# Performance work log

Measured on AMD Instinct MI355X. Metric: run time of the kernel, lower is better.

Reference implementation:

```python
import jax, jax.numpy as jnp
import numpy as np
from jax import lax

DIM = 1024
DIM_INNER = 2048  # int(dim * expansion_factor)


def log_g(x):
    # log-space g(x): where(x>=0, log(relu(x)+0.5), -softplus(-x))
    return jnp.where(x >= 0, jnp.log(jax.nn.relu(x) + 0.5), -jax.nn.softplus(-x))


def heinsen_associative_scan_log(log_coeffs, log_values):
    # parallel log-space linear recurrence over the sequence axis (axis=1)
    a_star = jnp.cumsum(log_coeffs, axis=1)
    log_h0_plus_b_star = lax.cumlogsumexp(log_values - a_star, axis=1)
    return a_star + log_h0_plus_b_star


def setup_inputs() -> dict:
    key = jax.random.key(0)
    k_x, k_w1, k_w2 = jax.random.split(key, 3)
    x = jax.random.normal(k_x, (4, 4096, DIM), dtype=jnp.float32)
    # Linear(dim, 2*dim_inner, bias=False): store as [in, out] for x @ W
    W_hg = jax.random.normal(k_w1, (DIM, 2 * DIM_INNER), dtype=jnp.float32) * (1.0 / np.sqrt(DIM))
    W_out = jax.random.normal(k_w2, (DIM_INNER, DIM), dtype=jnp.float32) * (1.0 / np.sqrt(DIM_INNER))
    return {"x": x, "W_hg": W_hg, "W_out": W_out}


def reference(x, W_hg, W_out):
    # x: [b, s, dim]
    hg = jnp.einsum('bsd,de->bse', x, W_hg)  # [b, s, 2*dim_inner]
    hidden, gate = jnp.split(hg, 2, axis=-1)
    log_coeffs = -jax.nn.softplus(gate)        # log(1 - z)
    log_z = -jax.nn.softplus(-gate)            # log z
    log_values = log_z + log_g(hidden)
    log_h = heinsen_associative_scan_log(log_coeffs, log_values)  # [b, s, dim_inner]
    out = jnp.exp(log_h)
    return jnp.einsum('bse,ed->bsd', out, W_out)
```

## Files before the change

kernel.cpp:

```cpp
#include <hip/hip_runtime.h>
#include <cmath>

#define DIM 1024
#define DIM_INNER 2048
#define BATCH 4
#define SEQ 4096
#define MTOT (BATCH * SEQ)
#define CHUNK 32
#define NCHUNK (SEQ / CHUNK)

typedef __bf16 bf16x8 __attribute__((ext_vector_type(8)));
typedef short short8_t __attribute__((ext_vector_type(8)));
typedef float floatx4 __attribute__((ext_vector_type(4)));
typedef unsigned short u16x4 __attribute__((ext_vector_type(4)));
typedef unsigned int uint4_t __attribute__((ext_vector_type(4)));
typedef float float4_t __attribute__((ext_vector_type(4)));
typedef unsigned short ushort_t;

__device__ __forceinline__ unsigned short f2bf(float f) {
  unsigned int u = __builtin_bit_cast(unsigned int, f);
  u += 0x7fffu + ((u >> 16) & 1u);
  return (unsigned short)(u >> 16);
}
__device__ __forceinline__ float bflo2f(unsigned int u) {
  return __builtin_bit_cast(float, u << 16);
}
__device__ __forceinline__ float bfhi2f(unsigned int u) {
  return __builtin_bit_cast(float, u & 0xffff0000u);
}

__device__ __forceinline__ void lclv_fast(float h, float g, float& lc, float& lv) {
  float eg = __expf(-fabsf(g));
  float sp = fmaxf(g, 0.f) + __logf(1.f + eg);
  lc = -sp;
  float eh = __expf(h);
  float t  = (h >= 0.f) ? (h + 0.5f) : (1.f + eh);
  float lt = __logf(t);
  float lg = (h >= 0.f) ? lt : (h - lt);
  lv = g + lc + lg;
}
__device__ __forceinline__ float logaddexp_f(float a, float b) {
  float m = fmaxf(a, b);
  return m + __logf(1.f + __expf(-fabsf(a - b)));
}

__device__ __forceinline__ void async_copy16(const ushort_t* g, ushort_t* l) {
  __builtin_amdgcn_global_load_lds(
      (const __attribute__((address_space(1))) void*)g,
      (__attribute__((address_space(3))) void*)l, 16, 0, 0);
}

__global__ __launch_bounds__(256) void convert_f32_bf16(
    const float* __restrict__ src, ushort_t* __restrict__ dst) {
  int i = blockIdx.x * 256 + threadIdx.x;
  float4 v = ((const float4*)src)[i];
  u16x4 o = {f2bf(v.x), f2bf(v.y), f2bf(v.z), f2bf(v.w)};
  ((u16x4*)dst)[i] = o;
}

__global__ __launch_bounds__(256) void transpose_f32_bf16(
    const float* __restrict__ src, ushort_t* __restrict__ dst, int K, int N) {
  __shared__ float tile[32][33];
  int tx = threadIdx.x & 31, ty = threadIdx.x >> 5;
  int n0 = blockIdx.x * 32, k0 = blockIdx.y * 32;
#pragma unroll
  for (int i = 0; i < 4; i++) {
    int k = ty + i * 8;
    tile[k][tx] = src[(size_t)(k0 + k) * N + n0 + tx];
  }
  __syncthreads();
#pragma unroll
  for (int i = 0; i < 4; i++) {
    int r = ty + i * 8;
    dst[(size_t)(n0 + r) * K + k0 + tx] = f2bf(tile[tx][r]);
  }
}

#define G1_BK 64
#define G1_NT (DIM / G1_BK)

__global__ __launch_bounds__(512, 2) void gemm1_fused(
    const ushort_t* __restrict__ Xbf, const ushort_t* __restrict__ Wt,
    unsigned int* __restrict__ LCLV) {
  __shared__ __align__(16) ushort_t lds[81920];

  const int tid = threadIdx.x;
  const int wv = tid >> 6;
  const int lane = tid & 63;
  const int wr = wv >> 2;
  const int wc = wv & 3;
  const int l15 = lane & 15;
  const int quad = lane >> 4;
  const int n0 = blockIdx.x * 128;
  const int m0 = blockIdx.y * 256;

  floatx4 acc[8][4];
#pragma unroll
  for (int i = 0; i < 8; i++)
#pragma unroll
    for (int j = 0; j < 4; j++) acc[i][j] = (floatx4){0.f, 0.f, 0.f, 0.f};

  bf16x8 aF[4][2], bF[2][2];

  auto stageA = [&](int kt, int half, int buf) {
#pragma unroll
    for (int L = 0; L < 2; L++) {
      int e = L * 512 + tid;
      int row = e >> 3, slot = e & 7;
      const ushort_t* src = Xbf + (size_t)(m0 + half * 128 + row) * DIM +
                            kt * 64 + ((slot ^ (row & 7)) << 3);
      async_copy16(src, lds + (buf * 2 + half) * 8192 + e * 8);
    }
  };
  auto stageB = [&](int kt, int half, int buf) {
#pragma unroll
    for (int L = 0; L < 2; L++) {
      int e = L * 512 + tid;
      int row = e >> 3, slot = e & 7;
      int br = half * 128 + row;
      int grow = n0 + ((br >> 6) << 5) + (br & 31) + ((br & 32) ? DIM_INNER : 0);
      const ushort_t* src = Wt + (size_t)grow * DIM +
                            kt * 64 + ((slot ^ (row & 7)) << 3);
      async_copy16(src, lds + 49152 + (buf * 2 + half) * 8192 + e * 8);
    }
  };
  auto readA = [&](int buf, int mf, int ks) -> bf16x8 {
    int r = mf * 16 + l15;
    const ushort_t* p = lds + (buf * 2 + wr) * 8192 + r * 64 +
                        ((((ks << 2) | quad) ^ (r & 7)) << 3);
    return __builtin_bit_cast(bf16x8, *(const short8_t*)p);
  };
  auto readB = [&](int buf, int nf, int ks) -> bf16x8 {
    int br = wc * 64 + nf * 16 + l15;
    int half = br >> 7, r = br & 127;
    const ushort_t* p = lds + 49152 + (buf * 2 + half) * 8192 + r * 64 +
                        ((((ks << 2) | quad) ^ (r & 7)) << 3);
    return __builtin_bit_cast(bf16x8, *(const short8_t*)p);
  };
  auto mmaQ = [&](int mb, int nb) {
#pragma unroll
    for (int mf = 0; mf < 4; mf++)
#pragma unroll
      for (int nf = 0; nf < 2; nf++)
#pragma unroll
        for (int ks = 0; ks < 2; ks++)
          acc[mb + mf][nb + nf] = __builtin_amdgcn_mfma_f32_16x16x32_bf16(
              aF[mf][ks], bF[nf][ks], acc[mb + mf][nb + nf], 0, 0, 0);
  };

  stageA(0, 0, 0); stageA(0, 1, 0);
  stageB(0, 0, 0); stageB(0, 1, 0);
  stageA(1, 0, 1); stageA(1, 1, 1);
  asm volatile("s_waitcnt vmcnt(4)" ::: "memory");
  __builtin_amdgcn_s_barrier();

  int bufA = 0, bufB = 0, bufAn = 2, bufBn = 1;
  for (int u = 0; u < G1_NT; u++) {
    const int kb = (u + 1 < G1_NT) ? u + 1 : G1_NT - 1;
    const int ka = (u + 2 < G1_NT) ? u + 2 : G1_NT - 1;

#pragma unroll
    for (int mf = 0; mf < 4; mf++)
#pragma unroll
      for (int ks = 0; ks < 2; ks++) aF[mf][ks] = readA(bufA, mf, ks);
#pragma unroll
    for (int nf = 0; nf < 2; nf++)
#pragma unroll
      for (int ks = 0; ks < 2; ks++) bF[nf][ks] = readB(bufB, nf, ks);
    stageB(kb, 0, bufBn);
    __builtin_amdgcn_s_barrier();
    asm volatile("s_waitcnt lgkmcnt(0)" ::: "memory");
    __builtin_amdgcn_sched_barrier(0);
    __builtin_amdgcn_s_setprio(1);
    mmaQ(0, 0);
    __builtin_amdgcn_s_setprio(0);
    __builtin_amdgcn_s_barrier();

#pragma unroll
    for (int nf = 0; nf < 2; nf++)
#pragma unroll
      for (int ks = 0; ks < 2; ks++) bF[nf][ks] = readB(bufB, nf + 2, ks);
    stageB(kb, 1, bufBn);
    __builtin_amdgcn_s_barrier();
    asm volatile("s_waitcnt lgkmcnt(0)" ::: "memory");
    __builtin_amdgcn_sched_barrier(0);
    __builtin_amdgcn_s_setprio(1);
    mmaQ(0, 2);
    __builtin_amdgcn_s_setprio(0);
    __builtin_amdgcn_s_barrier();

#pragma unroll
    for (int mf = 0; mf < 4; mf++)
#pragma unroll
      for (int ks = 0; ks < 2; ks++) aF[mf][ks] = readA(bufA, mf + 4, ks);
    stageA(ka, 0, bufAn);
    __builtin_amdgcn_s_barrier();
    asm volatile("s_waitcnt lgkmcnt(0)" ::: "memory");
    __builtin_amdgcn_sched_barrier(0);
    __builtin_amdgcn_s_setprio(1);
    mmaQ(4, 2);
    __builtin_amdgcn_s_setprio(0);
    __builtin_amdgcn_s_barrier();

#pragma unroll
    for (int nf = 0; nf < 2; nf++)
#pragma unroll
      for (int ks = 0; ks < 2; ks++) bF[nf][ks] = readB(bufB, nf, ks);
    stageA(ka, 1, bufAn);
    asm volatile("s_waitcnt vmcnt(4)" ::: "memory");
    __builtin_amdgcn_s_barrier();
    asm volatile("s_waitcnt lgkmcnt(0)" ::: "memory");
    __builtin_amdgcn_sched_barrier(0);
    __builtin_amdgcn_s_setprio(1);
    mmaQ(4, 0);
    __builtin_amdgcn_s_setprio(0);
    __builtin_amdgcn_s_barrier();

    bufA = (bufA == 2) ? 0 : bufA + 1;
    bufAn = (bufAn == 2) ? 0 : bufAn + 1;
    bufB ^= 1; bufBn ^= 1;
  }

#pragma unroll
  for (int mf = 0; mf < 8; mf++)
#pragma unroll
    for (int j = 0; j < 2; j++) {
      int col = n0 + wc * 32 + j * 16 + l15;
#pragma unroll
      for (int r = 0; r < 4; r++) {
        int row = m0 + wr * 128 + mf * 16 + quad * 4 + r;
        float lc, lv;
        lclv_fast(acc[mf][j][r], acc[mf][j + 2][r], lc, lv);
        unsigned int pk = ((unsigned int)f2bf(lv) << 16) | (unsigned int)f2bf(lc);
        LCLV[(size_t)row * DIM_INNER + col] = pk;
      }
    }
}

__global__ __launch_bounds__(256) void scan_phase1(
    const unsigned int* __restrict__ LCLV,
    float* __restrict__ Asum, float* __restrict__ Lend, int nbch) {
  const int EQ = DIM_INNER / 4;
  int tid = blockIdx.x * 256 + threadIdx.x;
  int ep = tid % EQ;
  int tmp = tid / EQ;
  int c = tmp % NCHUNK;
  int bz = tmp / NCHUNK;
  size_t base4 = ((size_t)bz * SEQ + (size_t)c * CHUNK) * EQ + ep;
  const uint4_t* L4 = (const uint4_t*)LCLV;

  float4_t asum = {0.f, 0.f, 0.f, 0.f};
  float4_t logh = {-INFINITY, -INFINITY, -INFINITY, -INFINITY};
#pragma unroll 4
  for (int t = 0; t < CHUNK; t++) {
    uint4_t u = L4[base4 + (size_t)t * EQ];
#pragma unroll
    for (int k = 0; k < 4; k++) {
      float lc = bflo2f(u[k]), lv = bfhi2f(u[k]);
      asum[k] += lc;
      logh[k] = logaddexp_f(lc + logh[k], lv);
    }
  }
  size_t sidx = ((size_t)c * nbch + (size_t)bz * DIM_INNER) / 4 + ep;
  ((float4_t*)Asum)[sidx] = asum;
  ((float4_t*)Lend)[sidx] = logh;
}

__global__ __launch_bounds__(256) void scan_phase2(
    float* Asum, const float* __restrict__ Lend, int nbch) {
  int ch = blockIdx.x * 256 + threadIdx.x;
  float p = -INFINITY;
  for (int c = 0; c < NCHUNK; c++) {
    float a = Asum[(size_t)c * nbch + ch];
    float le = Lend[(size_t)c * nbch + ch];
    Asum[(size_t)c * nbch + ch] = p;
    p = logaddexp_f(a + p, le);
  }
}

__global__ __launch_bounds__(256) void scan_phase3(
    const unsigned int* __restrict__ LCLV, const float* __restrict__ P,
    ushort_t* __restrict__ H, int nbch) {
  const int EQ = DIM_INNER / 4;
  int tid = blockIdx.x * 256 + threadIdx.x;
  int ep = tid % EQ;
  int tmp = tid / EQ;
  int c = tmp % NCHUNK;
  int bz = tmp / NCHUNK;
  size_t base4 = ((size_t)bz * SEQ + (size_t)c * CHUNK) * EQ + ep;
  const uint4_t* L4 = (const uint4_t*)LCLV;
  u16x4* H4 = (u16x4*)H;

  size_t pidx = ((size_t)c * nbch + (size_t)bz * DIM_INNER) / 4 + ep;
  float4_t logh = ((const float4_t*)P)[pidx];
#pragma unroll 4
  for (int t = 0; t < CHUNK; t++) {
    uint4_t u = L4[base4 + (size_t)t * EQ];
    u16x4 hv;
#pragma unroll
    for (int k = 0; k < 4; k++) {
      float lc = bflo2f(u[k]), lv = bfhi2f(u[k]);
      logh[k] = logaddexp_f(lc + logh[k], lv);
      hv[k] = f2bf(__expf(logh[k]));
    }
    H4[base4 + (size_t)t * EQ] = hv;
  }
}

__global__ __launch_bounds__(256) void gemm2(
    const ushort_t* __restrict__ Hbf, const ushort_t* __restrict__ Wot,
    float* __restrict__ OUT) {
  __shared__ __align__(16) ushort_t As[128 * 32];
  __shared__ __align__(16) ushort_t Bs[128 * 32];

  const int tid = threadIdx.x;
  const int wave = tid >> 6;
  const int lane = tid & 63;
  const int n0 = blockIdx.x * 128;
  const int m0 = blockIdx.y * 128;
  const int l15 = lane & 15;
  const int quad = lane >> 4;
  const int wr = wave >> 1, wc = wave & 1;
  const int lrow = lane >> 2;
  const int lkof = (lane & 3) * 8;

  floatx4 acc[4][4];
#pragma unroll
  for (int i = 0; i < 4; i++)
#pragma unroll
    for (int j = 0; j < 4; j++) acc[i][j] = (floatx4){0.f, 0.f, 0.f, 0.f};

  for (int k0 = 0; k0 < DIM_INNER; k0 += 32) {
    __syncthreads();
#pragma unroll
    for (int p = 0; p < 2; p++) {
      int u = wave + p * 4;
      async_copy16(Hbf + (size_t)(m0 + u * 16 + lrow) * DIM_INNER + k0 + lkof,
                   As + u * 512);
      async_copy16(Wot + (size_t)(n0 + u * 16 + lrow) * DIM_INNER + k0 + lkof,
                   Bs + u * 512);
    }
    __syncthreads();

    bf16x8 af[4], bf[4];
#pragma unroll
    for (int i = 0; i < 4; i++) {
      short8_t sa = *(const short8_t*)(As + (size_t)(wr * 64 + i * 16 + l15) * 32 + quad * 8);
      af[i] = __builtin_bit_cast(bf16x8, sa);
      short8_t sb = *(const short8_t*)(Bs + (size_t)(wc * 64 + i * 16 + l15) * 32 + quad * 8);
      bf[i] = __builtin_bit_cast(bf16x8, sb);
    }
#pragma unroll
    for (int i = 0; i < 4; i++)
#pragma unroll
      for (int j = 0; j < 4; j++)
        acc[i][j] = __builtin_amdgcn_mfma_f32_16x16x32_bf16(af[i], bf[j], acc[i][j], 0, 0, 0);
  }

#pragma unroll
  for (int i = 0; i < 4; i++)
#pragma unroll
    for (int j = 0; j < 4; j++) {
      int col = n0 + wc * 64 + j * 16 + l15;
#pragma unroll
      for (int r = 0; r < 4; r++) {
        int row = m0 + wr * 64 + i * 16 + quad * 4 + r;
        OUT[(size_t)row * DIM + col] = acc[i][j][r];
      }
    }
}

extern "C" void kernel_launch(void* const* d_in, const int* in_sizes, int n_in,
                              void* d_out, int out_size, void* d_ws, size_t ws_size,
                              hipStream_t stream) {
  const float* X = (const float*)d_in[0];
  const float* Whg = (const float*)d_in[1];
  const float* Wout = (const float*)d_in[2];
  float* out = (float*)d_out;

  ushort_t* Xbf = (ushort_t*)d_ws;
  ushort_t* Whg_t = Xbf + (size_t)MTOT * DIM;
  ushort_t* Wout_t = Whg_t + (size_t)(2 * DIM_INNER) * DIM;
  char* pp = (char*)(Wout_t + (size_t)DIM * DIM_INNER);

  const size_t fixed_bytes = (size_t)MTOT * DIM * 2 +
                             (size_t)2 * DIM_INNER * DIM * 2 +
                             (size_t)DIM * DIM_INNER * 2;
  const size_t per_batch = (size_t)SEQ * DIM_INNER * 4 +
                           (size_t)SEQ * DIM_INNER * 2 +
                           2 * (size_t)DIM_INNER * NCHUNK * 4;
  int nb = 4;
  while (nb > 1 && fixed_bytes + (size_t)nb * per_batch > ws_size) nb >>= 1;
  const int npass = BATCH / nb;

  convert_f32_bf16<<<(MTOT * DIM / 4) / 256, 256, 0, stream>>>(X, Xbf);
  transpose_f32_bf16<<<dim3(2 * DIM_INNER / 32, DIM / 32), 256, 0, stream>>>(
      Whg, Whg_t, DIM, 2 * DIM_INNER);
  transpose_f32_bf16<<<dim3(DIM / 32, DIM_INNER / 32), 256, 0, stream>>>(
      Wout, Wout_t, DIM_INNER, DIM);

  for (int pass = 0; pass < npass; pass++) {
    const int b0 = pass * nb;
    const int nrows = nb * SEQ;
    const int nbch = nb * DIM_INNER;

    unsigned int* LCLV = (unsigned int*)pp;
    ushort_t* Hbf = (ushort_t*)(LCLV + (size_t)nb * SEQ * DIM_INNER);
    float* Asum = (float*)(Hbf + (size_t)nb * SEQ * DIM_INNER);
    float* Lend = Asum + (size_t)nb * DIM_INNER * NCHUNK;

    gemm1_fused<<<dim3(DIM_INNER / 128, nrows / 256), 512, 0, stream>>>(
        Xbf + (size_t)b0 * SEQ * DIM, Whg_t, LCLV);
    scan_phase1<<<(nbch / 4 * NCHUNK) / 256, 256, 0, stream>>>(LCLV, Asum, Lend, nbch);
    scan_phase2<<<nbch / 256, 256, 0, stream>>>(Asum, Lend, nbch);
    scan_phase3<<<(nbch / 4 * NCHUNK) / 256, 256, 0, stream>>>(LCLV, Asum, Hbf, nbch);
    gemm2<<<dim3(DIM / 128, nrows / 128), 256, 0, stream>>>(
        Hbf, Wout_t, out + (size_t)b0 * SEQ * DIM);
  }
}
```

Before: 493.0 us.

## Pipeline GEMM1 LDS reads with incremental waits and rebuild GEMM2 on same schedule

GEMM1's main loop now precomputes global and LDS addresses. It splits fragment loads so MFMAs start after partial lgkmcnt waits instead of draining all LDS reads, and peels the last two iterations to drop redundant prefetches. GEMM2 is rewritten from a simple single-buffered 128x128 kernel into a 256x256, 512-thread, multi-buffered swizzled kernel that reuses the same schedule. This raises data reuse and overlaps memory with compute. The cost is higher register and LDS pressure and fewer blocks for GEMM2.

```diff
diff --git a/kernel.cpp b/kernel.cpp
--- a/kernel.cpp
+++ b/kernel.cpp
@@ -16,6 +16,14 @@
 typedef unsigned int uint4_t __attribute__((ext_vector_type(4)));
 typedef float float4_t __attribute__((ext_vector_type(4)));
 typedef unsigned short ushort_t;
+
+template <int N> struct IC { static constexpr int v = N; };
+template <bool B> struct BC { static constexpr bool v = B; };
+
+#define LGKM_SB(n) do { asm volatile("s_waitcnt lgkmcnt(" #n ")" ::: "memory"); \
+                        __builtin_amdgcn_sched_barrier(0); } while (0)
+#define SCHED0() __builtin_amdgcn_sched_barrier(0)
+#define SBAR() __builtin_amdgcn_s_barrier()
 
 __device__ __forceinline__ unsigned short f2bf(float f) {
   unsigned int u = __builtin_bit_cast(unsigned int, f);
@@ -76,8 +84,8 @@
   }
 }
 
-#define G1_BK 64
-#define G1_NT (DIM / G1_BK)
+#define G1_NT (DIM / 64)
+#define G2_NT (DIM_INNER / 64)
 
 __global__ __launch_bounds__(512, 2) void gemm1_fused(
     const ushort_t* __restrict__ Xbf, const ushort_t* __restrict__ Wt,
@@ -94,132 +102,163 @@
   const int n0 = blockIdx.x * 128;
   const int m0 = blockIdx.y * 256;
 
-  floatx4 acc[8][4];
-#pragma unroll
-  for (int i = 0; i < 8; i++)
-#pragma unroll
-    for (int j = 0; j < 4; j++) acc[i][j] = (floatx4){0.f, 0.f, 0.f, 0.f};
-
-  bf16x8 aF[4][2], bF[2][2];
-
-  auto stageA = [&](int kt, int half, int buf) {
-#pragma unroll
-    for (int L = 0; L < 2; L++) {
-      int e = L * 512 + tid;
-      int row = e >> 3, slot = e & 7;
-      const ushort_t* src = Xbf + (size_t)(m0 + half * 128 + row) * DIM +
-                            kt * 64 + ((slot ^ (row & 7)) << 3);
-      async_copy16(src, lds + (buf * 2 + half) * 8192 + e * 8);
-    }
-  };
-  auto stageB = [&](int kt, int half, int buf) {
-#pragma unroll
-    for (int L = 0; L < 2; L++) {
-      int e = L * 512 + tid;
-      int row = e >> 3, slot = e & 7;
+  int aSrc[2][2], bSrc[2][2];
+  int dstE[2];
+#pragma unroll
+  for (int L = 0; L < 2; L++) {
+    int e = L * 512 + tid;
+    int row = e >> 3, slot = e & 7;
+    int sw = (slot ^ (row & 7)) << 3;
+    dstE[L] = e * 8;
+#pragma unroll
+    for (int half = 0; half < 2; half++) {
+      aSrc[half][L] = (m0 + half * 128 + row) * DIM + sw;
       int br = half * 128 + row;
       int grow = n0 + ((br >> 6) << 5) + (br & 31) + ((br & 32) ? DIM_INNER : 0);
-      const ushort_t* src = Wt + (size_t)grow * DIM +
-                            kt * 64 + ((slot ^ (row & 7)) << 3);
-      async_copy16(src, lds + 49152 + (buf * 2 + half) * 8192 + e * 8);
-    }
-  };
+      bSrc[half][L] = grow * DIM + sw;
+    }
+  }
+
+  auto stageA = [&](int kt, int half, int buf) {
+#pragma unroll
+    for (int L = 0; L < 2; L++)
+      async_copy16(Xbf + aSrc[half][L] + kt * 64,
+                   lds + buf * 16384 + half * 8192 + dstE[L]);
+  };
+  auto stageB = [&](int kt, int half, int buf) {
+#pragma unroll
+    for (int L = 0; L < 2; L++)
+      async_copy16(Wt + bSrc[half][L] + kt * 64,
+                   lds + 49152 + buf * 16384 + half * 8192 + dstE[L]);
+  };
+
+  const int swz0 = ((quad ^ (l15 & 7)) << 3);
+  const int swz1 = (((4 | quad) ^ (l15 & 7)) << 3);
+  const int aB0 = wr * 8192 + l15 * 64 + swz0;
+  const int aB1 = wr * 8192 + l15 * 64 + swz1;
+  const int bB0 = wc * 4096 + l15 * 64 + swz0;
+  const int bB1 = wc * 4096 + l15 * 64 + swz1;
+
   auto readA = [&](int buf, int mf, int ks) -> bf16x8 {
-    int r = mf * 16 + l15;
-    const ushort_t* p = lds + (buf * 2 + wr) * 8192 + r * 64 +
-                        ((((ks << 2) | quad) ^ (r & 7)) << 3);
+    const ushort_t* p = lds + buf * 16384 + (ks ? aB1 : aB0) + mf * 1024;
     return __builtin_bit_cast(bf16x8, *(const short8_t*)p);
   };
   auto readB = [&](int buf, int nf, int ks) -> bf16x8 {
-    int br = wc * 64 + nf * 16 + l15;
-    int half = br >> 7, r = br & 127;
-    const ushort_t* p = lds + 49152 + (buf * 2 + half) * 8192 + r * 64 +
-                        ((((ks << 2) | quad) ^ (r & 7)) << 3);
+    const ushort_t* p = lds + 49152 + buf * 16384 + (ks ? bB1 : bB0) + nf * 1024;
     return __builtin_bit_cast(bf16x8, *(const short8_t*)p);
   };
-  auto mmaQ = [&](int mb, int nb) {
-#pragma unroll
-    for (int mf = 0; mf < 4; mf++)
-#pragma unroll
-      for (int nf = 0; nf < 2; nf++)
-#pragma unroll
-        for (int ks = 0; ks < 2; ks++)
-          acc[mb + mf][nb + nf] = __builtin_amdgcn_mfma_f32_16x16x32_bf16(
-              aF[mf][ks], bF[nf][ks], acc[mb + mf][nb + nf], 0, 0, 0);
-  };
-
+
+  floatx4 acc[8][4];
+#pragma unroll
+  for (int i = 0; i < 8; i++)
+#pragma unroll
+    for (int j = 0; j < 4; j++) acc[i][j] = (floatx4){0.f, 0.f, 0.f, 0.f};
+
+  bf16x8 aF[4][2], b0F[2][2], b1F[2][2];
+
+  auto mma4 = [&](auto MA, auto MC, auto J, bf16x8 (&bX)[2][2]) {
+#pragma unroll
+    for (int jj = 0; jj < 2; jj++)
+#pragma unroll
+      for (int ks = 0; ks < 2; ks++)
+        acc[MC.v][J.v + jj] = __builtin_amdgcn_mfma_f32_16x16x32_bf16(
+            aF[MA.v][ks], bX[jj][ks], acc[MC.v][J.v + jj], 0, 0, 0);
+  };
+  auto mmaRow = [&](auto J, bf16x8 (&bvec)[2]) {
+#pragma unroll
+    for (int m = 0; m < 4; m++)
+#pragma unroll
+      for (int ks = 0; ks < 2; ks++)
+        acc[m][J.v] = __builtin_amdgcn_mfma_f32_16x16x32_bf16(
+            aF[m][ks], bvec[ks], acc[m][J.v], 0, 0, 0);
+  };
+
+  int bufA = 0, bufB = 0, bufAn = 2, bufBn = 1;
+
+  auto tileBody = [&](int kb, int ka, auto STB, auto STA, auto VMALL) {
+    aF[0][0] = readA(bufA, 0, 0); aF[0][1] = readA(bufA, 0, 1);
+    b0F[0][0] = readB(bufB, 0, 0); b0F[0][1] = readB(bufB, 0, 1);
+    b0F[1][0] = readB(bufB, 1, 0); b0F[1][1] = readB(bufB, 1, 1);
+    SCHED0();
+    aF[1][0] = readA(bufA, 1, 0); aF[1][1] = readA(bufA, 1, 1);
+    SCHED0();
+    aF[2][0] = readA(bufA, 2, 0); aF[2][1] = readA(bufA, 2, 1);
+    SCHED0();
+    aF[3][0] = readA(bufA, 3, 0); aF[3][1] = readA(bufA, 3, 1);
+    SCHED0();
+    if constexpr (STB.v) stageB(kb, 0, bufBn);
+    SBAR();
+    __builtin_amdgcn_s_setprio(1);
+    LGKM_SB(6); mma4(IC<0>{}, IC<0>{}, IC<0>{}, b0F);
+    LGKM_SB(4); mma4(IC<1>{}, IC<1>{}, IC<0>{}, b0F);
+    LGKM_SB(2); mma4(IC<2>{}, IC<2>{}, IC<0>{}, b0F);
+    LGKM_SB(0); mma4(IC<3>{}, IC<3>{}, IC<0>{}, b0F);
+    __builtin_amdgcn_s_setprio(0);
+    SBAR();
+
+    b1F[0][0] = readB(bufB, 2, 0); b1F[0][1] = readB(bufB, 2, 1);
+    SCHED0();
+    b1F[1][0] = readB(bufB, 3, 0); b1F[1][1] = readB(bufB, 3, 1);
+    SCHED0();
+    if constexpr (STB.v) stageB(kb, 1, bufBn);
+    SBAR();
+    __builtin_amdgcn_s_setprio(1);
+    LGKM_SB(2); mmaRow(IC<2>{}, b1F[0]);
+    LGKM_SB(0); mmaRow(IC<3>{}, b1F[1]);
+    __builtin_amdgcn_s_setprio(0);
+    SBAR();
+
+    aF[0][0] = readA(bufA, 4, 0); aF[0][1] = readA(bufA, 4, 1);
+    SCHED0();
+    aF[1][0] = readA(bufA, 5, 0); aF[1][1] = readA(bufA, 5, 1);
+    SCHED0();
+    aF[2][0] = readA(bufA, 6, 0); aF[2][1] = readA(bufA, 6, 1);
+    SCHED0();
+    aF[3][0] = readA(bufA, 7, 0); aF[3][1] = readA(bufA, 7, 1);
+    SCHED0();
+    if constexpr (STA.v) stageA(ka, 0, bufAn);
+    SBAR();
+    __builtin_amdgcn_s_setprio(1);
+    LGKM_SB(6); mma4(IC<0>{}, IC<4>{}, IC<2>{}, b1F);
+    LGKM_SB(4); mma4(IC<1>{}, IC<5>{}, IC<2>{}, b1F);
+    LGKM_SB(2); mma4(IC<2>{}, IC<6>{}, IC<2>{}, b1F);
+    LGKM_SB(0); mma4(IC<3>{}, IC<7>{}, IC<2>{}, b1F);
+    __builtin_amdgcn_s_setprio(0);
+    SBAR();
+
+    if constexpr (STA.v) stageA(ka, 1, bufAn);
+    SCHED0();
+    if constexpr (STA.v) {
+      asm volatile("s_waitcnt vmcnt(4)" ::: "memory");
+    } else if constexpr (VMALL.v) {
+      asm volatile("s_waitcnt vmcnt(0)" ::: "memory");
+    }
+    SBAR();
+    __builtin_amdgcn_s_setprio(1);
+    mma4(IC<0>{}, IC<4>{}, IC<0>{}, b0F);
+    mma4(IC<1>{}, IC<5>{}, IC<0>{}, b0F);
+    mma4(IC<2>{}, IC<6>{}, IC<0>{}, b0F);
+    mma4(IC<3>{}, IC<7>{}, IC<0>{}, b0F);
+    __builtin_amdgcn_s_setprio(0);
+    SBAR();
+  };
+
+  stageB(0, 0, 0); stageB(0, 1, 0);
   stageA(0, 0, 0); stageA(0, 1, 0);
-  stageB(0, 0, 0); stageB(0, 1, 0);
   stageA(1, 0, 1); stageA(1, 1, 1);
   asm volatile("s_waitcnt vmcnt(4)" ::: "memory");
-  __builtin_amdgcn_s_barrier();
-
-  int bufA = 0, bufB = 0, bufAn = 2, bufBn = 1;
-  for (int u = 0; u < G1_NT; u++) {
-    const int kb = (u + 1 < G1_NT) ? u + 1 : G1_NT - 1;
-    const int ka = (u + 2 < G1_NT) ? u + 2 : G1_NT - 1;
-
-#pragma unroll
-    for (int mf = 0; mf < 4; mf++)
-#pragma unroll
-      for (int ks = 0; ks < 2; ks++) aF[mf][ks] = readA(bufA, mf, ks);
-#pragma unroll
-    for (int nf = 0; nf < 2; nf++)
-#pragma unroll
-      for (int ks = 0; ks < 2; ks++) bF[nf][ks] = readB(bufB, nf, ks);
-    stageB(kb, 0, bufBn);
-    __builtin_amdgcn_s_barrier();
-    asm volatile("s_waitcnt lgkmcnt(0)" ::: "memory");
-    __builtin_amdgcn_sched_barrier(0);
-    __builtin_amdgcn_s_setprio(1);
-    mmaQ(0, 0);
-    __builtin_amdgcn_s_setprio(0);
-    __builtin_amdgcn_s_barrier();
-
-#pragma unroll
-    for (int nf = 0; nf < 2; nf++)
-#pragma unroll
-      for (int ks = 0; ks < 2; ks++) bF[nf][ks] = readB(bufB, nf + 2, ks);
-    stageB(kb, 1, bufBn);
-    __builtin_amdgcn_s_barrier();
-    asm volatile("s_waitcnt lgkmcnt(0)" ::: "memory");
-    __builtin_amdgcn_sched_barrier(0);
-    __builtin_amdgcn_s_setprio(1);
-    mmaQ(0, 2);
-    __builtin_amdgcn_s_setprio(0);
-    __builtin_amdgcn_s_barrier();
-
-#pragma unroll
-    for (int mf = 0; mf < 4; mf++)
-#pragma unroll
-      for (int ks = 0; ks < 2; ks++) aF[mf][ks] = readA(bufA, mf + 4, ks);
-    stageA(ka, 0, bufAn);
-    __builtin_amdgcn_s_barrier();
-    asm volatile("s_waitcnt lgkmcnt(0)" ::: "memory");
-    __builtin_amdgcn_sched_barrier(0);
-    __builtin_amdgcn_s_setprio(1);
-    mmaQ(4, 2);
-    __builtin_amdgcn_s_setprio(0);
-    __builtin_amdgcn_s_barrier();
-
-#pragma unroll
-    for (int nf = 0; nf < 2; nf++)
-#pragma unroll
-      for (int ks = 0; ks < 2; ks++) bF[nf][ks] = readB(bufB, nf, ks);
-    stageA(ka, 1, bufAn);
-    asm volatile("s_waitcnt vmcnt(4)" ::: "memory");
-    __builtin_amdgcn_s_barrier();
-    asm volatile("s_waitcnt lgkmcnt(0)" ::: "memory");
-    __builtin_amdgcn_sched_barrier(0);
-    __builtin_amdgcn_s_setprio(1);
-    mmaQ(4, 0);
-    __builtin_amdgcn_s_setprio(0);
-    __builtin_amdgcn_s_barrier();
-
+  SBAR();
+
+  for (int u = 0; u < G1_NT - 2; u++) {
+    tileBody(u + 1, u + 2, BC<true>{}, BC<true>{}, BC<false>{});
     bufA = (bufA == 2) ? 0 : bufA + 1;
     bufAn = (bufAn == 2) ? 0 : bufAn + 1;
     bufB ^= 1; bufBn ^= 1;
   }
+  tileBody(G1_NT - 1, 0, BC<true>{}, BC<false>{}, BC<true>{});
+  bufA = (bufA == 2) ? 0 : bufA + 1;
+  bufB ^= 1;
+  tileBody(0, 0, BC<false>{}, BC<false>{}, BC<false>{});
 
 #pragma unroll
   for (int mf = 0; mf < 8; mf++)
@@ -233,6 +272,190 @@
         lclv_fast(acc[mf][j][r], acc[mf][j + 2][r], lc, lv);
         unsigned int pk = ((unsigned int)f2bf(lv) << 16) | (unsigned int)f2bf(lc);
         LCLV[(size_t)row * DIM_INNER + col] = pk;
+      }
+    }
+}
+
+__global__ __launch_bounds__(512, 2) void gemm2(
+    const ushort_t* __restrict__ Hbf, const ushort_t* __restrict__ Wot,
+    float* __restrict__ OUT) {
+  __shared__ __align__(16) ushort_t lds[81920];
+
+  const int tid = threadIdx.x;
+  const int wv = tid >> 6;
+  const int lane = tid & 63;
+  const int wr = wv >> 2;
+  const int wc = wv & 3;
+  const int l15 = lane & 15;
+  const int quad = lane >> 4;
+  const int n0 = blockIdx.x * 256;
+  const int m0 = blockIdx.y * 256;
+
+  int aSrc[2][2], bSrc[2][2];
+  int dstE[2];
+#pragma unroll
+  for (int L = 0; L < 2; L++) {
+    int e = L * 512 + tid;
+    int row = e >> 3, slot = e & 7;
+    int sw = (slot ^ (row & 7)) << 3;
+    dstE[L] = e * 8;
+#pragma unroll
+    for (int half = 0; half < 2; half++) {
+      aSrc[half][L] = (m0 + half * 128 + row) * DIM_INNER + sw;
+      bSrc[half][L] = (n0 + half * 128 + row) * DIM_INNER + sw;
+    }
+  }
+
+  auto stageA = [&](int kt, int half, int buf) {
+#pragma unroll
+    for (int L = 0; L < 2; L++)
+      async_copy16(Hbf + aSrc[half][L] + kt * 64,
+                   lds + buf * 16384 + half * 8192 + dstE[L]);
+  };
+  auto stageB = [&](int kt, int half, int buf) {
+#pragma unroll
+    for (int L = 0; L < 2; L++)
+      async_copy16(Wot + bSrc[half][L] + kt * 64,
+                   lds + 49152 + buf * 16384 + half * 8192 + dstE[L]);
+  };
+
+  const int swz0 = ((quad ^ (l15 & 7)) << 3);
+  const int swz1 = (((4 | quad) ^ (l15 & 7)) << 3);
+  const int aB0 = wr * 8192 + l15 * 64 + swz0;
+  const int aB1 = wr * 8192 + l15 * 64 + swz1;
+  const int bB0 = wc * 4096 + l15 * 64 + swz0;
+  const int bB1 = wc * 4096 + l15 * 64 + swz1;
+
+  auto readA = [&](int buf, int mf, int ks) -> bf16x8 {
+    const ushort_t* p = lds + buf * 16384 + (ks ? aB1 : aB0) + mf * 1024;
+    return __builtin_bit_cast(bf16x8, *(const short8_t*)p);
+  };
+  auto readB = [&](int buf, int nf, int ks) -> bf16x8 {
+    const ushort_t* p = lds + 49152 + buf * 16384 + (ks ? bB1 : bB0) + nf * 1024;
+    return __builtin_bit_cast(bf16x8, *(const short8_t*)p);
+  };
+
+  floatx4 acc[8][4];
+#pragma unroll
+  for (int i = 0; i < 8; i++)
+#pragma unroll
+    for (int j = 0; j < 4; j++) acc[i][j] = (floatx4){0.f, 0.f, 0.f, 0.f};
+
+  bf16x8 aF[4][2], b0F[2][2], b1F[2][2];
+
+  auto mma4 = [&](auto MA, auto MC, auto J, bf16x8 (&bX)[2][2]) {
+#pragma unroll
+    for (int jj = 0; jj < 2; jj++)
+#pragma unroll
+      for (int ks = 0; ks < 2; ks++)
+        acc[MC.v][J.v + jj] = __builtin_amdgcn_mfma_f32_16x16x32_bf16(
+            aF[MA.v][ks], bX[jj][ks], acc[MC.v][J.v + jj], 0, 0, 0);
+  };
+  auto mmaRow = [&](auto J, bf16x8 (&bvec)[2]) {
+#pragma unroll
+    for (int m = 0; m < 4; m++)
+#pragma unroll
+      for (int ks = 0; ks < 2; ks++)
+        acc[m][J.v] = __builtin_amdgcn_mfma_f32_16x16x32_bf16(
+            aF[m][ks], bvec[ks], acc[m][J.v], 0, 0, 0);
+  };
+
+  int bufA = 0, bufB = 0, bufAn = 2, bufBn = 1;
+
+  auto tileBody = [&](int kb, int ka, auto STB, auto STA, auto VMALL) {
+    aF[0][0] = readA(bufA, 0, 0); aF[0][1] = readA(bufA, 0, 1);
+    b0F[0][0] = readB(bufB, 0, 0); b0F[0][1] = readB(bufB, 0, 1);
+    b0F[1][0] = readB(bufB, 1, 0); b0F[1][1] = readB(bufB, 1, 1);
+    SCHED0();
+    aF[1][0] = readA(bufA, 1, 0); aF[1][1] = readA(bufA, 1, 1);
+    SCHED0();
+    aF[2][0] = readA(bufA, 2, 0); aF[2][1] = readA(bufA, 2, 1);
+    SCHED0();
+    aF[3][0] = readA(bufA, 3, 0); aF[3][1] = readA(bufA, 3, 1);
+    SCHED0();
+    if constexpr (STB.v) stageB(kb, 0, bufBn);
+    SBAR();
+    __builtin_amdgcn_s_setprio(1);
+    LGKM_SB(6); mma4(IC<0>{}, IC<0>{}, IC<0>{}, b0F);
+    LGKM_SB(4); mma4(IC<1>{}, IC<1>{}, IC<0>{}, b0F);
+    LGKM_SB(2); mma4(IC<2>{}, IC<2>{}, IC<0>{}, b0F);
+    LGKM_SB(0); mma4(IC<3>{}, IC<3>{}, IC<0>{}, b0F);
+    __builtin_amdgcn_s_setprio(0);
+    SBAR();
+
+    b1F[0][0] = readB(bufB, 2, 0); b1F[0][1] = readB(bufB, 2, 1);
+    SCHED0();
+    b1F[1][0] = readB(bufB, 3, 0); b1F[1][1] = readB(bufB, 3, 1);
+    SCHED0();
+    if constexpr (STB.v) stageB(kb, 1, bufBn);
+    SBAR();
+    __builtin_amdgcn_s_setprio(1);
+    LGKM_SB(2); mmaRow(IC<2>{}, b1F[0]);
+    LGKM_SB(0); mmaRow(IC<3>{}, b1F[1]);
+    __builtin_amdgcn_s_setprio(0);
+    SBAR();
+
+    aF[0][0] = readA(bufA, 4, 0); aF[0][1] = readA(bufA, 4, 1);
+    SCHED0();
+    aF[1][0] = readA(bufA, 5, 0); aF[1][1] = readA(bufA, 5, 1);
+    SCHED0();
+    aF[2][0] = readA(bufA, 6, 0); aF[2][1] = readA(bufA, 6, 1);
+    SCHED0();
+    aF[3][0] = readA(bufA, 7, 0); aF[3][1] = readA(bufA, 7, 1);
+    SCHED0();
+    if constexpr (STA.v) stageA(ka, 0, bufAn);
+    SBAR();
+    __builtin_amdgcn_s_setprio(1);
+    LGKM_SB(6); mma4(IC<0>{}, IC<4>{}, IC<2>{}, b1F);
+    LGKM_SB(4); mma4(IC<1>{}, IC<5>{}, IC<2>{}, b1F);
+    LGKM_SB(2); mma4(IC<2>{}, IC<6>{}, IC<2>{}, b1F);
+    LGKM_SB(0); mma4(IC<3>{}, IC<7>{}, IC<2>{}, b1F);
+    __builtin_amdgcn_s_setprio(0);
+    SBAR();
+
+    if constexpr (STA.v) stageA(ka, 1, bufAn);
+    SCHED0();
+    if constexpr (STA.v) {
+      asm volatile("s_waitcnt vmcnt(4)" ::: "memory");
+    } else if constexpr (VMALL.v) {
+      asm volatile("s_waitcnt vmcnt(0)" ::: "memory");
+    }
+    SBAR();
+    __builtin_amdgcn_s_setprio(1);
+    mma4(IC<0>{}, IC<4>{}, IC<0>{}, b0F);
+    mma4(IC<1>{}, IC<5>{}, IC<0>{}, b0F);
+    mma4(IC<2>{}, IC<6>{}, IC<0>{}, b0F);
+    mma4(IC<3>{}, IC<7>{}, IC<0>{}, b0F);
+    __builtin_amdgcn_s_setprio(0);
+    SBAR();
+  };
+
+  stageB(0, 0, 0); stageB(0, 1, 0);
+  stageA(0, 0, 0); stageA(0, 1, 0);
+  stageA(1, 0, 1); stageA(1, 1, 1);
+  asm volatile("s_waitcnt vmcnt(4)" ::: "memory");
+  SBAR();
+
+  for (int u = 0; u < G2_NT - 2; u++) {
+    tileBody(u + 1, u + 2, BC<true>{}, BC<true>{}, BC<false>{});
+    bufA = (bufA == 2) ? 0 : bufA + 1;
+    bufAn = (bufAn == 2) ? 0 : bufAn + 1;
+    bufB ^= 1; bufBn ^= 1;
+  }
+  tileBody(G2_NT - 1, 0, BC<true>{}, BC<false>{}, BC<true>{});
+  bufA = (bufA == 2) ? 0 : bufA + 1;
+  bufB ^= 1;
+  tileBody(0, 0, BC<false>{}, BC<false>{}, BC<false>{});
+
+#pragma unroll
+  for (int mf = 0; mf < 8; mf++)
+#pragma unroll
+    for (int j = 0; j < 4; j++) {
+      int col = n0 + wc * 64 + (j >> 1) * 32 + (j & 1) * 16 + l15;
+#pragma unroll
+      for (int r = 0; r < 4; r++) {
+        int row = m0 + wr * 128 + mf * 16 + quad * 4 + r;
+        OUT[(size_t)row * DIM + col] = acc[mf][j][r];
       }
     }
 }
@@ -307,69 +530,6 @@
   }
 }
 
-__global__ __launch_bounds__(256) void gemm2(
-    const ushort_t* __restrict__ Hbf, const ushort_t* __restrict__ Wot,
-    float* __restrict__ OUT) {
-  __shared__ __align__(16) ushort_t As[128 * 32];
-  __shared__ __align__(16) ushort_t Bs[128 * 32];
-
-  const int tid = threadIdx.x;
-  const int wave = tid >> 6;
-  const int lane = tid & 63;
-  const int n0 = blockIdx.x * 128;
-  const int m0 = blockIdx.y * 128;
-  const int l15 = lane & 15;
-  const int quad = lane >> 4;
-  const int wr = wave >> 1, wc = wave & 1;
-  const int lrow = lane >> 2;
-  const int lkof = (lane & 3) * 8;
-
-  floatx4 acc[4][4];
-#pragma unroll
-  for (int i = 0; i < 4; i++)
-#pragma unroll
-    for (int j = 0; j < 4; j++) acc[i][j] = (floatx4){0.f, 0.f, 0.f, 0.f};
-
-  for (int k0 = 0; k0 < DIM_INNER; k0 += 32) {
-    __syncthreads();
-#pragma unroll
-    for (int p = 0; p < 2; p++) {
-      int u = wave + p * 4;
-      async_copy16(Hbf + (size_t)(m0 + u * 16 + lrow) * DIM_INNER + k0 + lkof,
-                   As + u * 512);
-      async_copy16(Wot + (size_t)(n0 + u * 16 + lrow) * DIM_INNER + k0 + lkof,
-                   Bs + u * 512);
-    }
-    __syncthreads();
-
-    bf16x8 af[4], bf[4];
-#pragma unroll
-    for (int i = 0; i < 4; i++) {
-      short8_t sa = *(const short8_t*)(As + (size_t)(wr * 64 + i * 16 + l15) * 32 + quad * 8);
-      af[i] = __builtin_bit_cast(bf16x8, sa);
-      short8_t sb = *(const short8_t*)(Bs + (size_t)(wc * 64 + i * 16 + l15) * 32 + quad * 8);
-      bf[i] = __builtin_bit_cast(bf16x8, sb);
-    }
-#pragma unroll
-    for (int i = 0; i < 4; i++)
-#pragma unroll
-      for (int j = 0; j < 4; j++)
-        acc[i][j] = __builtin_amdgcn_mfma_f32_16x16x32_bf16(af[i], bf[j], acc[i][j], 0, 0, 0);
-  }
-
-#pragma unroll
-  for (int i = 0; i < 4; i++)
-#pragma unroll
-    for (int j = 0; j < 4; j++) {
-      int col = n0 + wc * 64 + j * 16 + l15;
-#pragma unroll
-      for (int r = 0; r < 4; r++) {
-        int row = m0 + wr * 64 + i * 16 + quad * 4 + r;
-        OUT[(size_t)row * DIM + col] = acc[i][j][r];
-      }
-    }
-}
-
 extern "C" void kernel_launch(void* const* d_in, const int* in_sizes, int n_in,
                               void* d_out, int out_size, void* d_ws, size_t ws_size,
                               hipStream_t stream) {
@@ -414,7 +574,7 @@
     scan_phase1<<<(nbch / 4 * NCHUNK) / 256, 256, 0, stream>>>(LCLV, Asum, Lend, nbch);
     scan_phase2<<<nbch / 256, 256, 0, stream>>>(Asum, Lend, nbch);
     scan_phase3<<<(nbch / 4 * NCHUNK) / 256, 256, 0, stream>>>(LCLV, Asum, Hbf, nbch);
-    gemm2<<<dim3(DIM / 128, nrows / 128), 256, 0, stream>>>(
+    gemm2<<<dim3(DIM / 256, nrows / 256), 512, 0, stream>>>(
         Hbf, Wout_t, out + (size_t)b0 * SEQ * DIM);
   }
 }
```

New measurement: 425.1 us. 13.8% less time.
